# Optimization experiments

Hardware: AMD Instinct MI355X
Metric: run time of the kernel (lower is better)

Reference implementation:

```python
import jax, jax.numpy as jnp
import numpy as np

N_NODES = 50000


def gcn_conv(x, W, b, src, dst, n_nodes):
    """PyG GCNConv: h = x @ W; symmetric-normalized aggregation with self-loops; + bias."""
    h = x @ W  # [N, F_out]
    ones = jnp.ones(src.shape[0], dtype=h.dtype)
    # degree including the self-loop (edge weight 1)
    deg = jax.ops.segment_sum(ones, dst, num_segments=n_nodes) + 1.0
    dinv = jax.lax.rsqrt(deg)  # deg >= 1, always valid
    norm = dinv[src] * dinv[dst]  # [E]
    msgs = h[src] * norm[:, None]  # [E, F_out]
    agg = jax.ops.segment_sum(msgs, dst, num_segments=n_nodes)
    agg = agg + h * (dinv * dinv)[:, None]  # self-loop contribution, norm = dinv_i^2
    return agg + b


def setup_inputs() -> dict:
    key = jax.random.key(0)
    ks = jax.random.split(key, 8)
    n, f_in, f_hid, f_out, n_edges = N_NODES, 128, 128, 40, 800000
    x = jax.random.normal(ks[0], (n, f_in), dtype=jnp.float32)
    edge_index = jax.random.randint(ks[1], (2, n_edges), 0, n, dtype=jnp.int64)
    new_edge_indexs = jax.random.randint(ks[2], (2, 1000), 0, n, dtype=jnp.int64)
    # Glorot init like PyG defaults
    s1 = (6.0 / (f_in + f_hid)) ** 0.5
    s2 = (6.0 / (f_hid + f_out)) ** 0.5
    W1 = jax.random.uniform(ks[3], (f_in, f_hid), jnp.float32, -s1, s1)
    b1 = jnp.zeros((f_hid,), jnp.float32)
    W2 = jax.random.uniform(ks[4], (f_hid, f_out), jnp.float32, -s2, s2)
    b2 = jnp.zeros((f_out,), jnp.float32)
    return {"x": x, "W1": W1, "b1": b1, "W2": W2, "b2": b2,
            "edge_index": edge_index, "new_edge_indexs": new_edge_indexs}


def reference(x, W1, b1, W2, b2, edge_index, new_edge_indexs):
    src, dst = edge_index[0], edge_index[1]
    h = gcn_conv(x, W1, b1, src, dst, N_NODES)
    h = jax.nn.relu(h)
    # dropout(p=0.5) is identity in eval mode (training=False)
    h = gcn_conv(h, W2, b2, src, dst, N_NODES)
    return jax.nn.log_softmax(h, axis=-1)
```

## Files before the change

### kernel.cpp

```cpp
#include <hip/hip_runtime.h>
#include <hip/hip_bf16.h>

#define N_NODES 50000
#define N_EDGES 800000
#define F_IN    128
#define F_HID   128
#define F_OUT   40
#define N_TILES (N_NODES / 16)

#define NBIN      98
#define BIN_SHIFT 9
#define EPB       1024
#define CAP       32
#define GBIN_CAP  9216

#define CVT_BLOCKS ((F_IN * F_HID + 48 * F_HID) / 256)
#define BIN_BLOCKS ((N_EDGES + EPB - 1) / EPB)
#define G1_BLOCKS  ((N_TILES + 3) / 4)

typedef __attribute__((ext_vector_type(8))) short bf16x8;
typedef __attribute__((ext_vector_type(4))) float f32x4;

__device__ __forceinline__ float2 unpack_bf2(unsigned u) {
    float2 r;
    r.x = __uint_as_float(u << 16);
    r.y = __uint_as_float(u & 0xffff0000u);
    return r;
}
__device__ __forceinline__ unsigned pack_bf2(float x, float y) {
    union { unsigned u; __hip_bfloat16 h[2]; } cv;
    cv.h[0] = __float2bfloat16(x);
    cv.h[1] = __float2bfloat16(y);
    return cv.u;
}
__device__ __forceinline__ short bfraw(float v) {
    __hip_bfloat16 h = __float2bfloat16(v);
    return *(short*)&h;
}
__device__ __forceinline__ float bf16u_to_f32(unsigned short us) {
    return __uint_as_float(((unsigned)us) << 16);
}
__device__ __forceinline__ unsigned f32_to_h16(float v) {
    _Float16 h = (_Float16)v;
    return (unsigned)*(unsigned short*)&h;
}
__device__ __forceinline__ float h16_to_f32(unsigned bits) {
    unsigned short us = (unsigned short)bits;
    _Float16 h = *(_Float16*)&us;
    return (float)h;
}

__device__ __forceinline__ int ld_src(const unsigned int* w, int is64, int e) {
    return is64 ? (int)w[2 * e] : (int)w[e];
}
__device__ __forceinline__ int ld_dst(const unsigned int* w, int is64, int e) {
    return is64 ? (int)w[2 * (N_EDGES + e)] : (int)w[N_EDGES + e];
}

__global__ void k_init(const unsigned int* __restrict__ ew,
                       const float* __restrict__ W1, const float* __restrict__ W2,
                       __hip_bfloat16* __restrict__ w1t, __hip_bfloat16* __restrict__ w2t,
                       int* __restrict__ flag, int* __restrict__ gcnt) {
    int b = blockIdx.x, t = threadIdx.x;
    if (b < CVT_BLOCKS) {
        int idx = b * 256 + t;
        if (idx < F_IN * F_HID) {
            int n = idx >> 7, k = idx & 127;
            w1t[idx] = __float2bfloat16(W1[k * F_HID + n]);
        } else {
            int j = idx - F_IN * F_HID;
            int n = j >> 7, k = j & 127;
            w2t[j] = __float2bfloat16(n < F_OUT ? W2[k * F_OUT + n] : 0.f);
        }
        return;
    }
    __shared__ int nz;
    if (t == 0) nz = 0;
    __syncthreads();
    int local = 0;
    for (int i = t; i < 4096; i += 256)
        if (ew[2 * i + 1] != 0u) local = 1;
    if (local) atomicOr(&nz, 1);
    if (t < NBIN) gcnt[t] = 0;
    __syncthreads();
    if (t == 0) flag[0] = (nz == 0) ? 1 : 0;
}

__global__ void k_bing1(const unsigned int* __restrict__ ew, const int* __restrict__ flag,
                        int* __restrict__ gcnt, unsigned* __restrict__ gbin,
                        const float* __restrict__ x, const __hip_bfloat16* __restrict__ w1t,
                        __hip_bfloat16* __restrict__ h1b) {
    __shared__ unsigned buf[NBIN][CAP];
    __shared__ int cnt[NBIN];
    __shared__ int base[NBIN];
    int t = threadIdx.x;
    if (blockIdx.x < BIN_BLOCKS) {
        for (int i = t; i < NBIN; i += 256) cnt[i] = 0;
        __syncthreads();
        int is64 = flag[0];
        int e0 = blockIdx.x * EPB;
        int n = min(EPB, N_EDGES - e0);
        for (int i = t; i < n; i += 256) {
            int e = e0 + i;
            int s = ld_src(ew, is64, e), d = ld_dst(ew, is64, e);
            unsigned rec = (unsigned)s | ((unsigned)d << 16);
            int b = d >> BIN_SHIFT;
            int c = atomicAdd(&cnt[b], 1);
            if (c < CAP) buf[b][c] = rec;
            else {
                int g = atomicAdd(&gcnt[b], 1);
                gbin[(size_t)b * GBIN_CAP + g] = rec;
            }
        }
        __syncthreads();
        if (t < NBIN) {
            int m = min(cnt[t], CAP);
            base[t] = atomicAdd(&gcnt[t], m);
            cnt[t] = m;
        }
        __syncthreads();
        int wave = t >> 6, lane = t & 63;
        for (int b = wave; b < NBIN; b += 4) {
            int m = cnt[b], bs = base[b];
            for (int i = lane; i < m; i += 64)
                gbin[(size_t)b * GBIN_CAP + bs + i] = buf[b][i];
        }
        return;
    }
    int wave = t >> 6, lane = t & 63;
    int tile = (blockIdx.x - BIN_BLOCKS) * 4 + wave;
    if (tile >= N_TILES) return;
    int node0 = tile * 16;
    int m = lane & 15, q = lane >> 4;
    bf16x8 A[4];
    const float* arow = x + (size_t)(node0 + m) * F_IN + q * 8;
#pragma unroll
    for (int kt = 0; kt < 4; kt++) {
        float4 f0 = *(const float4*)(arow + kt * 32);
        float4 f1 = *(const float4*)(arow + kt * 32 + 4);
        bf16x8 a;
        a[0] = bfraw(f0.x); a[1] = bfraw(f0.y); a[2] = bfraw(f0.z); a[3] = bfraw(f0.w);
        a[4] = bfraw(f1.x); a[5] = bfraw(f1.y); a[6] = bfraw(f1.z); a[7] = bfraw(f1.w);
        A[kt] = a;
    }
#pragma unroll
    for (int c = 0; c < 8; c++) {
        f32x4 acc = {0.f, 0.f, 0.f, 0.f};
        const __hip_bfloat16* brow = w1t + (size_t)(c * 16 + m) * F_IN + q * 8;
#pragma unroll
        for (int kt = 0; kt < 4; kt++) {
            bf16x8 B = *(const bf16x8*)(brow + kt * 32);
            acc = __builtin_amdgcn_mfma_f32_16x16x32_bf16(A[kt], B, acc, 0, 0, 0);
        }
#pragma unroll
        for (int r = 0; r < 4; r++)
            h1b[(size_t)(node0 + q * 4 + r) * F_HID + c * 16 + m] = __float2bfloat16(acc[r]);
    }
}

__global__ void k_passB1(const int* __restrict__ gcnt, const unsigned* __restrict__ gbin,
                         int* __restrict__ rowptr, float* __restrict__ dinv) {
    __shared__ int c[512];
    __shared__ int s2[256];
    __shared__ int gall[NBIN];
    __shared__ int bbase;
    int t = threadIdx.x;
    int b = blockIdx.x;
    c[t] = 0; c[t + 256] = 0;
    if (t < NBIN) gall[t] = gcnt[t];
    __syncthreads();
    if (t == 0) {
        int s = 0;
        for (int i = 0; i < b; i++) s += gall[i];
        bbase = s;
    }
    int n = gall[b];
    const unsigned* rec = gbin + (size_t)b * GBIN_CAP;
    int base512 = b << BIN_SHIFT;
    for (int i = t; i < n; i += 256)
        atomicAdd(&c[(int)(rec[i] >> 16) - base512], 1);
    __syncthreads();
    int a0 = c[2 * t], a1 = c[2 * t + 1];
    s2[t] = a0 + a1;
    __syncthreads();
    for (int off = 1; off < 256; off <<= 1) {
        int u = (t >= off) ? s2[t - off] : 0;
        __syncthreads();
        s2[t] += u;
        __syncthreads();
    }
    int ebase = bbase + s2[t] - a0 - a1;
    int i0 = base512 + 2 * t, i1 = i0 + 1;
    if (i0 < N_NODES) { rowptr[i0] = ebase;      dinv[i0] = rsqrtf((float)a0 + 1.f); }
    if (i1 < N_NODES) { rowptr[i1] = ebase + a0; dinv[i1] = rsqrtf((float)a1 + 1.f); }
    if (b == 0 && t == 0) rowptr[N_NODES] = N_EDGES;
}

__global__ void k_passB2(const int* __restrict__ gcnt, const unsigned* __restrict__ gbin,
                         const int* __restrict__ rowptr, const float* __restrict__ dinv,
                         unsigned* __restrict__ srcw) {
    __shared__ int pos[512];
    __shared__ float dloc[512];
    int t = threadIdx.x;
    int b = blockIdx.x;
    int base512 = b << BIN_SHIFT;
#pragma unroll
    for (int k = 0; k < 2; k++) {
        int j = t + k * 256;
        int i = base512 + j;
        pos[j]  = (i < N_NODES) ? rowptr[i] : 0;
        dloc[j] = (i < N_NODES) ? dinv[i] : 0.f;
    }
    __syncthreads();
    int n = gcnt[b];
    const unsigned* rec = gbin + (size_t)b * GBIN_CAP;
    for (int i = t; i < n; i += 256) {
        unsigned r = rec[i];
        int s  = (int)(r & 0xFFFFu);
        int dl = (int)(r >> 16) - base512;
        int slot = atomicAdd(&pos[dl], 1);
        float norm = dinv[s] * dloc[dl];
        srcw[slot] = (unsigned)s | (f32_to_h16(norm) << 16);
    }
}

__global__ void k_agg1f(const int* __restrict__ rowptr, const unsigned* __restrict__ srcw,
                        const float* __restrict__ dinv, const __hip_bfloat16* __restrict__ h1b,
                        const float* __restrict__ b1, __hip_bfloat16* __restrict__ h1rb) {
    int wave = threadIdx.x >> 6, lane = threadIdx.x & 63;
    int node = blockIdx.x * 4 + wave;
    float di = dinv[node];
    int beg = __builtin_amdgcn_readfirstlane(rowptr[node]);
    int end = __builtin_amdgcn_readfirstlane(rowptr[node + 1]);
    const unsigned* h1u = (const unsigned*)h1b;
    float2 acc = unpack_bf2(h1u[(size_t)node * 64 + lane]);
    float w0 = di * di;
    acc.x *= w0; acc.y *= w0;
    int e = beg;
    for (; e + 7 < end; e += 8) {
        unsigned p[8];
#pragma unroll
        for (int j = 0; j < 8; j++) p[j] = srcw[e + j];
        unsigned u[8];
#pragma unroll
        for (int j = 0; j < 8; j++)
            u[j] = h1u[(size_t)(p[j] & 0xFFFFu) * 64 + lane];
#pragma unroll
        for (int j = 0; j < 8; j++) {
            float w = h16_to_f32(p[j] >> 16);
            float2 v = unpack_bf2(u[j]);
            acc.x += v.x * w;
            acc.y += v.y * w;
        }
    }
    for (; e < end; e++) {
        unsigned p = srcw[e];
        float w = h16_to_f32(p >> 16);
        float2 v = unpack_bf2(h1u[(size_t)(p & 0xFFFFu) * 64 + lane]);
        acc.x += v.x * w;
        acc.y += v.y * w;
    }
    float2 bb = ((const float2*)b1)[lane];
    acc.x = fmaxf(acc.x + bb.x, 0.f);
    acc.y = fmaxf(acc.y + bb.y, 0.f);
    ((unsigned*)h1rb)[(size_t)node * 64 + lane] = pack_bf2(acc.x, acc.y);
}

__global__ void k_gemm2m(const __hip_bfloat16* __restrict__ h1rb,
                         const __hip_bfloat16* __restrict__ w2t,
                         __hip_bfloat16* __restrict__ h2b) {
    int wave = threadIdx.x >> 6, lane = threadIdx.x & 63;
    int tile = blockIdx.x * 4 + wave;
    if (tile >= N_TILES) return;
    int node0 = tile * 16;
    int m = lane & 15, q = lane >> 4;
    bf16x8 A[4];
    const __hip_bfloat16* arow = h1rb + (size_t)(node0 + m) * F_HID + q * 8;
#pragma unroll
    for (int kt = 0; kt < 4; kt++)
        A[kt] = *(const bf16x8*)(arow + kt * 32);
#pragma unroll
    for (int c = 0; c < 3; c++) {
        f32x4 acc = {0.f, 0.f, 0.f, 0.f};
        const __hip_bfloat16* brow = w2t + (size_t)(c * 16 + m) * F_HID + q * 8;
#pragma unroll
        for (int kt = 0; kt < 4; kt++) {
            bf16x8 B = *(const bf16x8*)(brow + kt * 32);
            acc = __builtin_amdgcn_mfma_f32_16x16x32_bf16(A[kt], B, acc, 0, 0, 0);
        }
        int col = c * 16 + m;
        if (col < F_OUT) {
#pragma unroll
            for (int r = 0; r < 4; r++)
                h2b[(size_t)(node0 + q * 4 + r) * F_OUT + col] = __float2bfloat16(acc[r]);
        }
    }
}

__global__ void k_agg2f(const int* __restrict__ rowptr, const unsigned* __restrict__ srcw,
                        const float* __restrict__ dinv,
                        const unsigned short* __restrict__ h2b,
                        const float* __restrict__ b2, float* __restrict__ out) {
    int wave = threadIdx.x >> 6, lane = threadIdx.x & 63;
    int node = blockIdx.x * 4 + wave;
    float di = dinv[node];
    int beg = __builtin_amdgcn_readfirstlane(rowptr[node]);
    int end = __builtin_amdgcn_readfirstlane(rowptr[node + 1]);
    int l = (lane < F_OUT) ? lane : 0;
    float acc = bf16u_to_f32(h2b[(size_t)node * F_OUT + l]) * di * di;
    int e = beg;
    for (; e + 7 < end; e += 8) {
        unsigned p[8];
#pragma unroll
        for (int j = 0; j < 8; j++) p[j] = srcw[e + j];
        float v[8];
#pragma unroll
        for (int j = 0; j < 8; j++)
            v[j] = bf16u_to_f32(h2b[(size_t)(p[j] & 0xFFFFu) * F_OUT + l]);
#pragma unroll
        for (int j = 0; j < 8; j++)
            acc += v[j] * h16_to_f32(p[j] >> 16);
    }
    for (; e < end; e++) {
        unsigned p = srcw[e];
        acc += bf16u_to_f32(h2b[(size_t)(p & 0xFFFFu) * F_OUT + l]) * h16_to_f32(p >> 16);
    }
    float v = (lane < F_OUT) ? acc + b2[lane] : -INFINITY;
    float m = v;
    for (int off = 32; off; off >>= 1) m = fmaxf(m, __shfl_xor(m, off));
    float ex = (lane < F_OUT) ? __expf(v - m) : 0.f;
    float ssum = ex;
    for (int off = 32; off; off >>= 1) ssum += __shfl_xor(ssum, off);
    float ls = __logf(ssum);
    if (lane < F_OUT)
        out[(size_t)node * F_OUT + lane] = v - m - ls;
}

extern "C" void kernel_launch(void* const* d_in, const int* in_sizes, int n_in,
                              void* d_out, int out_size, void* d_ws, size_t ws_size,
                              hipStream_t stream) {
    const float* x  = (const float*)d_in[0];
    const float* W1 = (const float*)d_in[1];
    const float* b1 = (const float*)d_in[2];
    const float* W2 = (const float*)d_in[3];
    const float* b2 = (const float*)d_in[4];
    const unsigned int* ew = (const unsigned int*)d_in[5];
    float* out = (float*)d_out;

    char* ws = (char*)d_ws;
    int*   flag     = (int*)ws;   ws += 256;
    int*   gcnt     = (int*)ws;   ws += 512;
    float* dinv     = (float*)ws; ws += ((N_NODES * 4 + 255) / 256) * 256;
    int*   rowptr   = (int*)ws;   ws += (((N_NODES + 1) * 4 + 255) / 256) * 256;
    unsigned* gbin  = (unsigned*)ws; ws += (size_t)NBIN * GBIN_CAP * 4;
    unsigned* srcw  = (unsigned*)ws; ws += (size_t)N_EDGES * 4;
    __hip_bfloat16* w1t  = (__hip_bfloat16*)ws; ws += F_IN * F_HID * 2;
    __hip_bfloat16* w2t  = (__hip_bfloat16*)ws; ws += 48 * F_HID * 2;
    __hip_bfloat16* h1b  = (__hip_bfloat16*)ws; ws += (size_t)N_NODES * F_HID * 2;
    __hip_bfloat16* h1rb = (__hip_bfloat16*)ws; ws += (size_t)N_NODES * F_HID * 2;
    __hip_bfloat16* h2b  = (__hip_bfloat16*)ws; ws += (size_t)N_NODES * F_OUT * 2;

    k_init   <<<CVT_BLOCKS + 1, 256, 0, stream>>>(ew, W1, W2, w1t, w2t, flag, gcnt);
    k_bing1  <<<BIN_BLOCKS + G1_BLOCKS, 256, 0, stream>>>(ew, flag, gcnt, gbin, x, w1t, h1b);
    k_passB1 <<<NBIN, 256, 0, stream>>>(gcnt, gbin, rowptr, dinv);
    k_passB2 <<<NBIN, 256, 0, stream>>>(gcnt, gbin, rowptr, dinv, srcw);
    k_agg1f  <<<N_NODES / 4, 256, 0, stream>>>(rowptr, srcw, dinv, h1b, b1, h1rb);
    k_gemm2m <<<(N_TILES + 3) / 4, 256, 0, stream>>>(h1rb, w2t, h2b);
    k_agg2f  <<<N_NODES / 4, 256, 0, stream>>>(rowptr, srcw, dinv,
                                               (const unsigned short*)h2b, b2, out);
}
```

Baseline: 212.2 us.

## Prescale features by dinv, fuse layer-1 aggregation with GEMM2, merge CSR passes

Node degrees are now counted with global atomics during binning, so one of the two CSR-building passes goes away and the GEMM1 moves into the scatter kernel. Features are prescaled by dinv of the source node after each GEMM, so edges store only the source index and aggregation becomes a plain sum followed by a multiply by dinv of the destination. Layer-1 aggregation is fused with the second GEMM through shared memory, which removes the h1rb round trip and one launch. The trade-off is extra global atomic traffic on deg and an added dependency of GEMM1 on the completed degree counts.

Result: slower. 219.9 us (+3.6%).

```diff
diff --git a/kernel.cpp b/kernel.cpp
--- a/kernel.cpp
+++ b/kernel.cpp
@@ -15,6 +15,7 @@
 #define GBIN_CAP  9216
 
 #define CVT_BLOCKS ((F_IN * F_HID + 48 * F_HID) / 256)
+#define DEGZ_BLOCKS 196
 #define BIN_BLOCKS ((N_EDGES + EPB - 1) / EPB)
 #define G1_BLOCKS  ((N_TILES + 3) / 4)
 
@@ -40,15 +41,6 @@
 __device__ __forceinline__ float bf16u_to_f32(unsigned short us) {
     return __uint_as_float(((unsigned)us) << 16);
 }
-__device__ __forceinline__ unsigned f32_to_h16(float v) {
-    _Float16 h = (_Float16)v;
-    return (unsigned)*(unsigned short*)&h;
-}
-__device__ __forceinline__ float h16_to_f32(unsigned bits) {
-    unsigned short us = (unsigned short)bits;
-    _Float16 h = *(_Float16*)&us;
-    return (float)h;
-}
 
 __device__ __forceinline__ int ld_src(const unsigned int* w, int is64, int e) {
     return is64 ? (int)w[2 * e] : (int)w[e];
@@ -60,7 +52,8 @@
 __global__ void k_init(const unsigned int* __restrict__ ew,
                        const float* __restrict__ W1, const float* __restrict__ W2,
                        __hip_bfloat16* __restrict__ w1t, __hip_bfloat16* __restrict__ w2t,
-                       int* __restrict__ flag, int* __restrict__ gcnt) {
+                       int* __restrict__ flag, int* __restrict__ gcnt,
+                       int* __restrict__ deg) {
     int b = blockIdx.x, t = threadIdx.x;
     if (b < CVT_BLOCKS) {
         int idx = b * 256 + t;
@@ -74,6 +67,11 @@
         }
         return;
     }
+    if (b < CVT_BLOCKS + DEGZ_BLOCKS) {
+        int i = (b - CVT_BLOCKS) * 256 + t;
+        if (i < N_NODES) deg[i] = 0;
+        return;
+    }
     __shared__ int nz;
     if (t == 0) nz = 0;
     __syncthreads();
@@ -86,52 +84,103 @@
     if (t == 0) flag[0] = (nz == 0) ? 1 : 0;
 }
 
-__global__ void k_bing1(const unsigned int* __restrict__ ew, const int* __restrict__ flag,
-                        int* __restrict__ gcnt, unsigned* __restrict__ gbin,
-                        const float* __restrict__ x, const __hip_bfloat16* __restrict__ w1t,
-                        __hip_bfloat16* __restrict__ h1b) {
+__global__ void k_bindeg(const unsigned int* __restrict__ ew, const int* __restrict__ flag,
+                         int* __restrict__ gcnt, unsigned* __restrict__ gbin,
+                         int* __restrict__ deg) {
     __shared__ unsigned buf[NBIN][CAP];
     __shared__ int cnt[NBIN];
     __shared__ int base[NBIN];
     int t = threadIdx.x;
-    if (blockIdx.x < BIN_BLOCKS) {
-        for (int i = t; i < NBIN; i += 256) cnt[i] = 0;
+    for (int i = t; i < NBIN; i += 256) cnt[i] = 0;
+    __syncthreads();
+    int is64 = flag[0];
+    int e0 = blockIdx.x * EPB;
+    int n = min(EPB, N_EDGES - e0);
+    for (int i = t; i < n; i += 256) {
+        int e = e0 + i;
+        int s = ld_src(ew, is64, e), d = ld_dst(ew, is64, e);
+        atomicAdd(&deg[d], 1);
+        unsigned rec = (unsigned)s | ((unsigned)d << 16);
+        int b = d >> BIN_SHIFT;
+        int c = atomicAdd(&cnt[b], 1);
+        if (c < CAP) buf[b][c] = rec;
+        else {
+            int g = atomicAdd(&gcnt[b], 1);
+            gbin[(size_t)b * GBIN_CAP + g] = rec;
+        }
+    }
+    __syncthreads();
+    if (t < NBIN) {
+        int m = min(cnt[t], CAP);
+        base[t] = atomicAdd(&gcnt[t], m);
+        cnt[t] = m;
+    }
+    __syncthreads();
+    int wave = t >> 6, lane = t & 63;
+    for (int b = wave; b < NBIN; b += 4) {
+        int m = cnt[b], bs = base[b];
+        for (int i = lane; i < m; i += 64)
+            gbin[(size_t)b * GBIN_CAP + bs + i] = buf[b][i];
+    }
+}
+
+__global__ void k_scatg1(const int* __restrict__ gcnt, const unsigned* __restrict__ gbin,
+                         const int* __restrict__ deg,
+                         int* __restrict__ rowptr, unsigned* __restrict__ srcw,
+                         const float* __restrict__ x, const __hip_bfloat16* __restrict__ w1t,
+                         __hip_bfloat16* __restrict__ h1b) {
+    __shared__ int pos[512];
+    __shared__ int s2[256];
+    __shared__ int gall[NBIN];
+    __shared__ int bbase;
+    int t = threadIdx.x;
+    if (blockIdx.x < NBIN) {
+        int b = blockIdx.x;
+        if (t < NBIN) gall[t] = gcnt[t];
+        int base512 = b << BIN_SHIFT;
+        int i0 = base512 + 2 * t, i1 = i0 + 1;
+        int d0 = (i0 < N_NODES) ? deg[i0] : 0;
+        int d1 = (i1 < N_NODES) ? deg[i1] : 0;
         __syncthreads();
-        int is64 = flag[0];
-        int e0 = blockIdx.x * EPB;
-        int n = min(EPB, N_EDGES - e0);
+        if (t == 0) {
+            int s = 0;
+            for (int i = 0; i < b; i++) s += gall[i];
+            bbase = s;
+        }
+        s2[t] = d0 + d1;
+        __syncthreads();
+        for (int off = 1; off < 256; off <<= 1) {
+            int u = (t >= off) ? s2[t - off] : 0;
+            __syncthreads();
+            s2[t] += u;
+            __syncthreads();
+        }
+        int ebase = bbase + s2[t] - d0 - d1;
+        if (i0 < N_NODES) rowptr[i0] = ebase;
+        if (i1 < N_NODES) rowptr[i1] = ebase + d0;
+        pos[2 * t] = ebase;
+        pos[2 * t + 1] = ebase + d0;
+        if (b == 0 && t == 0) rowptr[N_NODES] = N_EDGES;
+        __syncthreads();
+        int n = gall[b];
+        const unsigned* rec = gbin + (size_t)b * GBIN_CAP;
         for (int i = t; i < n; i += 256) {
-            int e = e0 + i;
-            int s = ld_src(ew, is64, e), d = ld_dst(ew, is64, e);
-            unsigned rec = (unsigned)s | ((unsigned)d << 16);
-            int b = d >> BIN_SHIFT;
-            int c = atomicAdd(&cnt[b], 1);
-            if (c < CAP) buf[b][c] = rec;
-            else {
-                int g = atomicAdd(&gcnt[b], 1);
-                gbin[(size_t)b * GBIN_CAP + g] = rec;
-            }
-        }
-        __syncthreads();
-        if (t < NBIN) {
-            int m = min(cnt[t], CAP);
-            base[t] = atomicAdd(&gcnt[t], m);
-            cnt[t] = m;
-        }
-        __syncthreads();
-        int wave = t >> 6, lane = t & 63;
-        for (int b = wave; b < NBIN; b += 4) {
-            int m = cnt[b], bs = base[b];
-            for (int i = lane; i < m; i += 64)
-                gbin[(size_t)b * GBIN_CAP + bs + i] = buf[b][i];
+            unsigned r = rec[i];
+            int dl = (int)(r >> 16) - base512;
+            int slot = atomicAdd(&pos[dl], 1);
+            srcw[slot] = r & 0xFFFFu;
         }
         return;
     }
     int wave = t >> 6, lane = t & 63;
-    int tile = (blockIdx.x - BIN_BLOCKS) * 4 + wave;
+    int tile = (blockIdx.x - NBIN) * 4 + wave;
     if (tile >= N_TILES) return;
     int node0 = tile * 16;
     int m = lane & 15, q = lane >> 4;
+    float dv[4];
+#pragma unroll
+    for (int r = 0; r < 4; r++)
+        dv[r] = rsqrtf((float)deg[node0 + q * 4 + r] + 1.f);
     bf16x8 A[4];
     const float* arow = x + (size_t)(node0 + m) * F_IN + q * 8;
 #pragma unroll
@@ -154,133 +203,64 @@
         }
 #pragma unroll
         for (int r = 0; r < 4; r++)
-            h1b[(size_t)(node0 + q * 4 + r) * F_HID + c * 16 + m] = __float2bfloat16(acc[r]);
-    }
-}
-
-__global__ void k_passB1(const int* __restrict__ gcnt, const unsigned* __restrict__ gbin,
-                         int* __restrict__ rowptr, float* __restrict__ dinv) {
-    __shared__ int c[512];
-    __shared__ int s2[256];
-    __shared__ int gall[NBIN];
-    __shared__ int bbase;
-    int t = threadIdx.x;
-    int b = blockIdx.x;
-    c[t] = 0; c[t + 256] = 0;
-    if (t < NBIN) gall[t] = gcnt[t];
-    __syncthreads();
-    if (t == 0) {
-        int s = 0;
-        for (int i = 0; i < b; i++) s += gall[i];
-        bbase = s;
-    }
-    int n = gall[b];
-    const unsigned* rec = gbin + (size_t)b * GBIN_CAP;
-    int base512 = b << BIN_SHIFT;
-    for (int i = t; i < n; i += 256)
-        atomicAdd(&c[(int)(rec[i] >> 16) - base512], 1);
-    __syncthreads();
-    int a0 = c[2 * t], a1 = c[2 * t + 1];
-    s2[t] = a0 + a1;
-    __syncthreads();
-    for (int off = 1; off < 256; off <<= 1) {
-        int u = (t >= off) ? s2[t - off] : 0;
-        __syncthreads();
-        s2[t] += u;
-        __syncthreads();
-    }
-    int ebase = bbase + s2[t] - a0 - a1;
-    int i0 = base512 + 2 * t, i1 = i0 + 1;
-    if (i0 < N_NODES) { rowptr[i0] = ebase;      dinv[i0] = rsqrtf((float)a0 + 1.f); }
-    if (i1 < N_NODES) { rowptr[i1] = ebase + a0; dinv[i1] = rsqrtf((float)a1 + 1.f); }
-    if (b == 0 && t == 0) rowptr[N_NODES] = N_EDGES;
-}
-
-__global__ void k_passB2(const int* __restrict__ gcnt, const unsigned* __restrict__ gbin,
-                         const int* __restrict__ rowptr, const float* __restrict__ dinv,
-                         unsigned* __restrict__ srcw) {
-    __shared__ int pos[512];
-    __shared__ float dloc[512];
-    int t = threadIdx.x;
-    int b = blockIdx.x;
-    int base512 = b << BIN_SHIFT;
-#pragma unroll
-    for (int k = 0; k < 2; k++) {
-        int j = t + k * 256;
-        int i = base512 + j;
-        pos[j]  = (i < N_NODES) ? rowptr[i] : 0;
-        dloc[j] = (i < N_NODES) ? dinv[i] : 0.f;
-    }
-    __syncthreads();
-    int n = gcnt[b];
-    const unsigned* rec = gbin + (size_t)b * GBIN_CAP;
-    for (int i = t; i < n; i += 256) {
-        unsigned r = rec[i];
-        int s  = (int)(r & 0xFFFFu);
-        int dl = (int)(r >> 16) - base512;
-        int slot = atomicAdd(&pos[dl], 1);
-        float norm = dinv[s] * dloc[dl];
-        srcw[slot] = (unsigned)s | (f32_to_h16(norm) << 16);
-    }
-}
-
-__global__ void k_agg1f(const int* __restrict__ rowptr, const unsigned* __restrict__ srcw,
-                        const float* __restrict__ dinv, const __hip_bfloat16* __restrict__ h1b,
-                        const float* __restrict__ b1, __hip_bfloat16* __restrict__ h1rb) {
-    int wave = threadIdx.x >> 6, lane = threadIdx.x & 63;
-    int node = blockIdx.x * 4 + wave;
-    float di = dinv[node];
-    int beg = __builtin_amdgcn_readfirstlane(rowptr[node]);
-    int end = __builtin_amdgcn_readfirstlane(rowptr[node + 1]);
+            h1b[(size_t)(node0 + q * 4 + r) * F_HID + c * 16 + m] =
+                __float2bfloat16(acc[r] * dv[r]);
+    }
+}
+
+__global__ void k_agg1g2(const int* __restrict__ rowptr, const unsigned* __restrict__ srcw,
+                         const int* __restrict__ deg, const __hip_bfloat16* __restrict__ h1b,
+                         const float* __restrict__ b1, const __hip_bfloat16* __restrict__ w2t,
+                         __hip_bfloat16* __restrict__ h2b) {
+    __shared__ __align__(16) short h1r[16][136];
+    __shared__ float dvs[16];
+    int t = threadIdx.x, wave = t >> 6, lane = t & 63;
+    int node0 = blockIdx.x * 16;
     const unsigned* h1u = (const unsigned*)h1b;
-    float2 acc = unpack_bf2(h1u[(size_t)node * 64 + lane]);
-    float w0 = di * di;
-    acc.x *= w0; acc.y *= w0;
-    int e = beg;
-    for (; e + 7 < end; e += 8) {
-        unsigned p[8];
-#pragma unroll
-        for (int j = 0; j < 8; j++) p[j] = srcw[e + j];
-        unsigned u[8];
-#pragma unroll
-        for (int j = 0; j < 8; j++)
-            u[j] = h1u[(size_t)(p[j] & 0xFFFFu) * 64 + lane];
-#pragma unroll
-        for (int j = 0; j < 8; j++) {
-            float w = h16_to_f32(p[j] >> 16);
-            float2 v = unpack_bf2(u[j]);
-            acc.x += v.x * w;
-            acc.y += v.y * w;
-        }
-    }
-    for (; e < end; e++) {
-        unsigned p = srcw[e];
-        float w = h16_to_f32(p >> 16);
-        float2 v = unpack_bf2(h1u[(size_t)(p & 0xFFFFu) * 64 + lane]);
-        acc.x += v.x * w;
-        acc.y += v.y * w;
-    }
-    float2 bb = ((const float2*)b1)[lane];
-    acc.x = fmaxf(acc.x + bb.x, 0.f);
-    acc.y = fmaxf(acc.y + bb.y, 0.f);
-    ((unsigned*)h1rb)[(size_t)node * 64 + lane] = pack_bf2(acc.x, acc.y);
-}
-
-__global__ void k_gemm2m(const __hip_bfloat16* __restrict__ h1rb,
-                         const __hip_bfloat16* __restrict__ w2t,
-                         __hip_bfloat16* __restrict__ h2b) {
-    int wave = threadIdx.x >> 6, lane = threadIdx.x & 63;
-    int tile = blockIdx.x * 4 + wave;
-    if (tile >= N_TILES) return;
-    int node0 = tile * 16;
-    int m = lane & 15, q = lane >> 4;
-    bf16x8 A[4];
-    const __hip_bfloat16* arow = h1rb + (size_t)(node0 + m) * F_HID + q * 8;
-#pragma unroll
-    for (int kt = 0; kt < 4; kt++)
-        A[kt] = *(const bf16x8*)(arow + kt * 32);
-#pragma unroll
-    for (int c = 0; c < 3; c++) {
+#pragma unroll
+    for (int i = 0; i < 4; i++) {
+        int row = wave * 4 + i;
+        int node = node0 + row;
+        float di = rsqrtf((float)deg[node] + 1.f);
+        int beg = __builtin_amdgcn_readfirstlane(rowptr[node]);
+        int end = __builtin_amdgcn_readfirstlane(rowptr[node + 1]);
+        float2 acc = unpack_bf2(h1u[(size_t)node * 64 + lane]);
+        int e = beg;
+        for (; e + 7 < end; e += 8) {
+            unsigned p[8];
+#pragma unroll
+            for (int j = 0; j < 8; j++) p[j] = srcw[e + j];
+            unsigned u[8];
+#pragma unroll
+            for (int j = 0; j < 8; j++)
+                u[j] = h1u[(size_t)p[j] * 64 + lane];
+#pragma unroll
+            for (int j = 0; j < 8; j++) {
+                float2 v = unpack_bf2(u[j]);
+                acc.x += v.x;
+                acc.y += v.y;
+            }
+        }
+        for (; e < end; e++) {
+            unsigned p = srcw[e];
+            float2 v = unpack_bf2(h1u[(size_t)p * 64 + lane]);
+            acc.x += v.x;
+            acc.y += v.y;
+        }
+        float2 bb = ((const float2*)b1)[lane];
+        acc.x = fmaxf(acc.x * di + bb.x, 0.f);
+        acc.y = fmaxf(acc.y * di + bb.y, 0.f);
+        ((unsigned*)&h1r[row][0])[lane] = pack_bf2(acc.x, acc.y);
+        if (lane == 0) dvs[row] = di;
+    }
+    __syncthreads();
+    if (wave < 3) {
+        int m = lane & 15, q = lane >> 4;
+        bf16x8 A[4];
+#pragma unroll
+        for (int kt = 0; kt < 4; kt++)
+            A[kt] = *(const bf16x8*)(&h1r[m][q * 8 + kt * 32]);
+        int c = wave;
         f32x4 acc = {0.f, 0.f, 0.f, 0.f};
         const __hip_bfloat16* brow = w2t + (size_t)(c * 16 + m) * F_HID + q * 8;
 #pragma unroll
@@ -292,22 +272,23 @@
         if (col < F_OUT) {
 #pragma unroll
             for (int r = 0; r < 4; r++)
-                h2b[(size_t)(node0 + q * 4 + r) * F_OUT + col] = __float2bfloat16(acc[r]);
+                h2b[(size_t)(node0 + q * 4 + r) * F_OUT + col] =
+                    __float2bfloat16(acc[r] * dvs[q * 4 + r]);
         }
     }
 }
 
 __global__ void k_agg2f(const int* __restrict__ rowptr, const unsigned* __restrict__ srcw,
-                        const float* __restrict__ dinv,
+                        const int* __restrict__ deg,
                         const unsigned short* __restrict__ h2b,
                         const float* __restrict__ b2, float* __restrict__ out) {
     int wave = threadIdx.x >> 6, lane = threadIdx.x & 63;
     int node = blockIdx.x * 4 + wave;
-    float di = dinv[node];
+    float di = rsqrtf((float)deg[node] + 1.f);
     int beg = __builtin_amdgcn_readfirstlane(rowptr[node]);
     int end = __builtin_amdgcn_readfirstlane(rowptr[node + 1]);
     int l = (lane < F_OUT) ? lane : 0;
-    float acc = bf16u_to_f32(h2b[(size_t)node * F_OUT + l]) * di * di;
+    float acc = bf16u_to_f32(h2b[(size_t)node * F_OUT + l]);
     int e = beg;
     for (; e + 7 < end; e += 8) {
         unsigned p[8];
@@ -316,16 +297,16 @@
         float v[8];
 #pragma unroll
         for (int j = 0; j < 8; j++)
-            v[j] = bf16u_to_f32(h2b[(size_t)(p[j] & 0xFFFFu) * F_OUT + l]);
+            v[j] = bf16u_to_f32(h2b[(size_t)p[j] * F_OUT + l]);
 #pragma unroll
         for (int j = 0; j < 8; j++)
-            acc += v[j] * h16_to_f32(p[j] >> 16);
+            acc += v[j];
     }
     for (; e < end; e++) {
         unsigned p = srcw[e];
-        acc += bf16u_to_f32(h2b[(size_t)(p & 0xFFFFu) * F_OUT + l]) * h16_to_f32(p >> 16);
-    }
-    float v = (lane < F_OUT) ? acc + b2[lane] : -INFINITY;
+        acc += bf16u_to_f32(h2b[(size_t)p * F_OUT + l]);
+    }
+    float v = (lane < F_OUT) ? acc * di + b2[lane] : -INFINITY;
     float m = v;
     for (int off = 32; off; off >>= 1) m = fmaxf(m, __shfl_xor(m, off));
     float ex = (lane < F_OUT) ? __expf(v - m) : 0.f;
@@ -350,22 +331,21 @@
     char* ws = (char*)d_ws;
     int*   flag     = (int*)ws;   ws += 256;
     int*   gcnt     = (int*)ws;   ws += 512;
-    float* dinv     = (float*)ws; ws += ((N_NODES * 4 + 255) / 256) * 256;
+    int*   deg      = (int*)ws;   ws += ((N_NODES * 4 + 255) / 256) * 256;
     int*   rowptr   = (int*)ws;   ws += (((N_NODES + 1) * 4 + 255) / 256) * 256;
     unsigned* gbin  = (unsigned*)ws; ws += (size_t)NBIN * GBIN_CAP * 4;
     unsigned* srcw  = (unsigned*)ws; ws += (size_t)N_EDGES * 4;
     __hip_bfloat16* w1t  = (__hip_bfloat16*)ws; ws += F_IN * F_HID * 2;
     __hip_bfloat16* w2t  = (__hip_bfloat16*)ws; ws += 48 * F_HID * 2;
     __hip_bfloat16* h1b  = (__hip_bfloat16*)ws; ws += (size_t)N_NODES * F_HID * 2;
-    __hip_bfloat16* h1rb = (__hip_bfloat16*)ws; ws += (size_t)N_NODES * F_HID * 2;
     __hip_bfloat16* h2b  = (__hip_bfloat16*)ws; ws += (size_t)N_NODES * F_OUT * 2;
 
-    k_init   <<<CVT_BLOCKS + 1, 256, 0, stream>>>(ew, W1, W2, w1t, w2t, flag, gcnt);
-    k_bing1  <<<BIN_BLOCKS + G1_BLOCKS, 256, 0, stream>>>(ew, flag, gcnt, gbin, x, w1t, h1b);
-    k_passB1 <<<NBIN, 256, 0, stream>>>(gcnt, gbin, rowptr, dinv);
-    k_passB2 <<<NBIN, 256, 0, stream>>>(gcnt, gbin, rowptr, dinv, srcw);
-    k_agg1f  <<<N_NODES / 4, 256, 0, stream>>>(rowptr, srcw, dinv, h1b, b1, h1rb);
-    k_gemm2m <<<(N_TILES + 3) / 4, 256, 0, stream>>>(h1rb, w2t, h2b);
-    k_agg2f  <<<N_NODES / 4, 256, 0, stream>>>(rowptr, srcw, dinv,
+    k_init   <<<CVT_BLOCKS + DEGZ_BLOCKS + 1, 256, 0, stream>>>(ew, W1, W2, w1t, w2t,
+                                                                flag, gcnt, deg);
+    k_bindeg <<<BIN_BLOCKS, 256, 0, stream>>>(ew, flag, gcnt, gbin, deg);
+    k_scatg1 <<<NBIN + G1_BLOCKS, 256, 0, stream>>>(gcnt, gbin, deg, rowptr, srcw,
+                                                    x, w1t, h1b);
+    k_agg1g2 <<<N_NODES / 16, 256, 0, stream>>>(rowptr, srcw, deg, h1b, b1, w2t, h2b);
+    k_agg2f  <<<N_NODES / 4, 256, 0, stream>>>(rowptr, srcw, deg,
                                                (const unsigned short*)h2b, b2, out);
 }
```

## Fuse layer-1 aggregation with layer-2 GEMM through shared memory

Applied to the files above, without the earlier changes.

Merges the first-layer neighbor aggregation (with bias and ReLU) and the second-layer MFMA GEMM into one kernel. Each block aggregates 16 nodes into an LDS tile, then three waves run the 16x48 MFMA directly from LDS. This removes the h1rb global round-trip (write plus read of 12.8 MB) and one kernel launch. In exchange each wave now processes 4 nodes serially, which lowers per-node parallelism, and one wave sits idle during the GEMM phase.

New measurement: 205.7 us. -3.1%, faster.

```diff
diff --git a/kernel.cpp b/kernel.cpp
--- a/kernel.cpp
+++ b/kernel.cpp
@@ -224,63 +224,61 @@
     }
 }
 
-__global__ void k_agg1f(const int* __restrict__ rowptr, const unsigned* __restrict__ srcw,
-                        const float* __restrict__ dinv, const __hip_bfloat16* __restrict__ h1b,
-                        const float* __restrict__ b1, __hip_bfloat16* __restrict__ h1rb) {
-    int wave = threadIdx.x >> 6, lane = threadIdx.x & 63;
-    int node = blockIdx.x * 4 + wave;
-    float di = dinv[node];
-    int beg = __builtin_amdgcn_readfirstlane(rowptr[node]);
-    int end = __builtin_amdgcn_readfirstlane(rowptr[node + 1]);
+__global__ void k_agg1g2(const int* __restrict__ rowptr, const unsigned* __restrict__ srcw,
+                         const float* __restrict__ dinv, const __hip_bfloat16* __restrict__ h1b,
+                         const float* __restrict__ b1, const __hip_bfloat16* __restrict__ w2t,
+                         __hip_bfloat16* __restrict__ h2b) {
+    __shared__ __align__(16) short h1r[16][136];
+    int t = threadIdx.x, wave = t >> 6, lane = t & 63;
+    int node0 = blockIdx.x * 16;
     const unsigned* h1u = (const unsigned*)h1b;
-    float2 acc = unpack_bf2(h1u[(size_t)node * 64 + lane]);
-    float w0 = di * di;
-    acc.x *= w0; acc.y *= w0;
-    int e = beg;
-    for (; e + 7 < end; e += 8) {
-        unsigned p[8];
-#pragma unroll
-        for (int j = 0; j < 8; j++) p[j] = srcw[e + j];
-        unsigned u[8];
-#pragma unroll
-        for (int j = 0; j < 8; j++)
-            u[j] = h1u[(size_t)(p[j] & 0xFFFFu) * 64 + lane];
-#pragma unroll
-        for (int j = 0; j < 8; j++) {
-            float w = h16_to_f32(p[j] >> 16);
-            float2 v = unpack_bf2(u[j]);
+#pragma unroll
+    for (int i = 0; i < 4; i++) {
+        int row = wave * 4 + i;
+        int node = node0 + row;
+        float di = dinv[node];
+        int beg = __builtin_amdgcn_readfirstlane(rowptr[node]);
+        int end = __builtin_amdgcn_readfirstlane(rowptr[node + 1]);
+        float2 acc = unpack_bf2(h1u[(size_t)node * 64 + lane]);
+        float w0 = di * di;
+        acc.x *= w0; acc.y *= w0;
+        int e = beg;
+        for (; e + 7 < end; e += 8) {
+            unsigned p[8];
+#pragma unroll
+            for (int j = 0; j < 8; j++) p[j] = srcw[e + j];
+            unsigned u[8];
+#pragma unroll
+            for (int j = 0; j < 8; j++)
+                u[j] = h1u[(size_t)(p[j] & 0xFFFFu) * 64 + lane];
+#pragma unroll
+            for (int j = 0; j < 8; j++) {
+                float w = h16_to_f32(p[j] >> 16);
+                float2 v = unpack_bf2(u[j]);
+                acc.x += v.x * w;
+                acc.y += v.y * w;
+            }
+        }
+        for (; e < end; e++) {
+            unsigned p = srcw[e];
+            float w = h16_to_f32(p >> 16);
+            float2 v = unpack_bf2(h1u[(size_t)(p & 0xFFFFu) * 64 + lane]);
             acc.x += v.x * w;
             acc.y += v.y * w;
         }
-    }
-    for (; e < end; e++) {
-        unsigned p = srcw[e];
-        float w = h16_to_f32(p >> 16);
-        float2 v = unpack_bf2(h1u[(size_t)(p & 0xFFFFu) * 64 + lane]);
-        acc.x += v.x * w;
-        acc.y += v.y * w;
-    }
-    float2 bb = ((const float2*)b1)[lane];
-    acc.x = fmaxf(acc.x + bb.x, 0.f);
-    acc.y = fmaxf(acc.y + bb.y, 0.f);
-    ((unsigned*)h1rb)[(size_t)node * 64 + lane] = pack_bf2(acc.x, acc.y);
-}
-
-__global__ void k_gemm2m(const __hip_bfloat16* __restrict__ h1rb,
-                         const __hip_bfloat16* __restrict__ w2t,
-                         __hip_bfloat16* __restrict__ h2b) {
-    int wave = threadIdx.x >> 6, lane = threadIdx.x & 63;
-    int tile = blockIdx.x * 4 + wave;
-    if (tile >= N_TILES) return;
-    int node0 = tile * 16;
-    int m = lane & 15, q = lane >> 4;
-    bf16x8 A[4];
-    const __hip_bfloat16* arow = h1rb + (size_t)(node0 + m) * F_HID + q * 8;
-#pragma unroll
-    for (int kt = 0; kt < 4; kt++)
-        A[kt] = *(const bf16x8*)(arow + kt * 32);
-#pragma unroll
-    for (int c = 0; c < 3; c++) {
+        float2 bb = ((const float2*)b1)[lane];
+        acc.x = fmaxf(acc.x + bb.x, 0.f);
+        acc.y = fmaxf(acc.y + bb.y, 0.f);
+        ((unsigned*)&h1r[row][0])[lane] = pack_bf2(acc.x, acc.y);
+    }
+    __syncthreads();
+    if (wave < 3) {
+        int m = lane & 15, q = lane >> 4;
+        bf16x8 A[4];
+#pragma unroll
+        for (int kt = 0; kt < 4; kt++)
+            A[kt] = *(const bf16x8*)(&h1r[m][q * 8 + kt * 32]);
+        int c = wave;
         f32x4 acc = {0.f, 0.f, 0.f, 0.f};
         const __hip_bfloat16* brow = w2t + (size_t)(c * 16 + m) * F_HID + q * 8;
 #pragma unroll
@@ -357,15 +355,13 @@
     __hip_bfloat16* w1t  = (__hip_bfloat16*)ws; ws += F_IN * F_HID * 2;
     __hip_bfloat16* w2t  = (__hip_bfloat16*)ws; ws += 48 * F_HID * 2;
     __hip_bfloat16* h1b  = (__hip_bfloat16*)ws; ws += (size_t)N_NODES * F_HID * 2;
-    __hip_bfloat16* h1rb = (__hip_bfloat16*)ws; ws += (size_t)N_NODES * F_HID * 2;
     __hip_bfloat16* h2b  = (__hip_bfloat16*)ws; ws += (size_t)N_NODES * F_OUT * 2;
 
     k_init   <<<CVT_BLOCKS + 1, 256, 0, stream>>>(ew, W1, W2, w1t, w2t, flag, gcnt);
     k_bing1  <<<BIN_BLOCKS + G1_BLOCKS, 256, 0, stream>>>(ew, flag, gcnt, gbin, x, w1t, h1b);
     k_passB1 <<<NBIN, 256, 0, stream>>>(gcnt, gbin, rowptr, dinv);
     k_passB2 <<<NBIN, 256, 0, stream>>>(gcnt, gbin, rowptr, dinv, srcw);
-    k_agg1f  <<<N_NODES / 4, 256, 0, stream>>>(rowptr, srcw, dinv, h1b, b1, h1rb);
-    k_gemm2m <<<(N_TILES + 3) / 4, 256, 0, stream>>>(h1rb, w2t, h2b);
+    k_agg1g2 <<<N_NODES / 16, 256, 0, stream>>>(rowptr, srcw, dinv, h1b, b1, w2t, h2b);
     k_agg2f  <<<N_NODES / 4, 256, 0, stream>>>(rowptr, srcw, dinv,
                                                (const unsigned short*)h2b, b2, out);
 }
```
